# Kernel optimization log

Hardware: AMD Instinct MI355X
Metric: run time of the kernel (lower is better)

Reference implementation:

```python
import jax, jax.numpy as jnp
import numpy as np

N_NODES = 50000
N_EDGES = 800000
IN_FEATS = 256
N_HIDDEN = 256
N_CLASSES = 47


def _glorot(key, shape):
    fan_in, fan_out = shape
    lim = (6.0 / (fan_in + fan_out)) ** 0.5
    return jax.random.uniform(key, shape, jnp.float32, -lim, lim)


def setup_inputs() -> dict:
    key = jax.random.key(0)
    ks = jax.random.split(key, 12)
    x = jax.random.normal(ks[0], (N_NODES, IN_FEATS), jnp.float32)
    src = jax.random.randint(ks[1], (N_EDGES,), 0, N_NODES, jnp.int64)
    dst = jax.random.randint(ks[2], (N_EDGES,), 0, N_NODES, jnp.int64)
    dims = [(IN_FEATS, N_HIDDEN), (N_HIDDEN, N_HIDDEN), (N_HIDDEN, N_CLASSES)]
    inp = {"x": x, "src": src, "dst": dst}
    for i, (di, do) in enumerate(dims):
        inp[f"Wself{i}"] = _glorot(ks[3 + 3 * i], (di, do))
        inp[f"Wneigh{i}"] = _glorot(ks[4 + 3 * i], (di, do))
        inp[f"b{i}"] = jnp.zeros((do,), jnp.float32)
    return inp


def _sage_layer(h, src, dst, Ws, Wn, b):
    # DGL mean SAGEConv: fc_self(h) + fc_neigh(mean over in-neighbors) + bias
    msum = jax.ops.segment_sum(h[src], dst, num_segments=N_NODES)      # [N, d]
    deg = jax.ops.segment_sum(jnp.ones((src.shape[0],), h.dtype), dst,
                              num_segments=N_NODES)                     # [N]
    hmean = msum / jnp.maximum(deg, 1.0)[:, None]
    return h @ Ws + hmean @ Wn + b


def reference(x, src, dst, Wself0, Wneigh0, b0, Wself1, Wneigh1, b1,
              Wself2, Wneigh2, b2):
    h = _sage_layer(x, src, dst, Wself0, Wneigh0, b0)
    h = jax.nn.selu(h)
    h = _sage_layer(h, src, dst, Wself1, Wneigh1, b1)
    h = jax.nn.selu(h)
    h = _sage_layer(h, src, dst, Wself2, Wneigh2, b2)
    return jax.nn.softmax(h, axis=1)
```

## Files before the change

kernel.cpp:

```cpp
#include <hip/hip_runtime.h>
#include <math.h>

#define FEATS 256
#define KTOT  512
#define MS    264
#define SA    40

typedef __attribute__((ext_vector_type(8))) __bf16 bf16x8;
typedef __attribute__((ext_vector_type(4))) float f32x4;

__device__ __forceinline__ float bf2f(unsigned short u) {
    union { unsigned int i; float f; } v; v.i = ((unsigned int)u) << 16; return v.f;
}
__device__ __forceinline__ unsigned short f2bf(float f) {
    unsigned int u = __float_as_uint(f);
    unsigned int r = (u + 0x7FFFu + ((u >> 16) & 1u)) >> 16;
    return (unsigned short)r;
}

__global__ void k_detect(const int* __restrict__ srcRaw, const unsigned short* __restrict__ xr,
                         int nE, int* __restrict__ flag) {
    __shared__ int any, cnt;
    if (threadIdx.x == 0) { any = 0; cnt = 0; }
    __syncthreads();
    int lim = nE < 1024 ? nE : 1024;
    for (int i = threadIdx.x; i < lim; i += 256)
        if (srcRaw[2 * i + 1] != 0) atomicAdd(&any, 1);
    int loc = 0;
    for (int i = threadIdx.x; i < 1024; i += 256) {
        unsigned e = (xr[2 * i] >> 7) & 255u;
        if (e >= 90u && e <= 140u) loc++;
    }
    atomicAdd(&cnt, loc);
    __syncthreads();
    if (threadIdx.x == 0) {
        flag[0] = (any == 0) ? 1 : 0;
        flag[1] = (cnt > 512) ? 1 : 0;
    }
}

__global__ void k_count(const int* __restrict__ dstRaw, int* __restrict__ deg, int nE,
                        int nNodes, const int* __restrict__ flag) {
    int e = blockIdx.x * 256 + threadIdx.x;
    if (e >= nE) return;
    int f = flag[0];
    int d = dstRaw[f ? (2 * e) : e];
    if ((unsigned)d >= (unsigned)nNodes) d = 0;
    atomicAdd(&deg[d], 1);
}

__global__ __launch_bounds__(256) void k_bsum(const int* __restrict__ deg, int* __restrict__ bsum,
                                              int n) {
    __shared__ int buf[256];
    const int t = threadIdx.x;
    int i = blockIdx.x * 256 + t;
    buf[t] = (i < n) ? deg[i] : 0;
    __syncthreads();
    for (int s = 128; s > 0; s >>= 1) {
        if (t < s) buf[t] += buf[t + s];
        __syncthreads();
    }
    if (t == 0) bsum[blockIdx.x] = buf[0];
}

__global__ __launch_bounds__(256) void k_scanb(int* __restrict__ bsum, int nB) {
    __shared__ int buf[256];
    __shared__ int carry;
    const int t = threadIdx.x;
    if (t == 0) carry = 0;
    __syncthreads();
    for (int base = 0; base < nB; base += 256) {
        int i = base + t;
        int v = (i < nB) ? bsum[i] : 0;
        buf[t] = v;
        __syncthreads();
        for (int s = 1; s < 256; s <<= 1) {
            int tv = (t >= s) ? buf[t - s] : 0;
            __syncthreads();
            buf[t] += tv;
            __syncthreads();
        }
        int exc = buf[t] - v;
        int c = carry;
        if (i < nB) bsum[i] = c + exc;
        int tot = buf[255];
        __syncthreads();
        if (t == 0) carry = c + tot;
        __syncthreads();
    }
}

__global__ __launch_bounds__(256) void k_offs(const int* __restrict__ deg,
                                              const int* __restrict__ bsum,
                                              int* __restrict__ off, int* __restrict__ cursor,
                                              int n) {
    __shared__ int buf[256];
    const int t = threadIdx.x, b = blockIdx.x;
    int i = b * 256 + t;
    int v = (i < n) ? deg[i] : 0;
    buf[t] = v;
    __syncthreads();
    for (int s = 1; s < 256; s <<= 1) {
        int tv = (t >= s) ? buf[t - s] : 0;
        __syncthreads();
        buf[t] += tv;
        __syncthreads();
    }
    int exc = bsum[b] + buf[t] - v;
    if (i < n) { off[i] = exc; cursor[i] = exc; }
    if (i == n - 1) off[n] = exc + v;
}

__global__ void k_fill(const int* __restrict__ srcRaw, const int* __restrict__ dstRaw,
                       int* __restrict__ cursor, int* __restrict__ csr, int nE,
                       int nNodes, const int* __restrict__ flag) {
    int e = blockIdx.x * 256 + threadIdx.x;
    if (e >= nE) return;
    int f = flag[0];
    int d = dstRaw[f ? (2 * e) : e];
    int s = srcRaw[f ? (2 * e) : e];
    if ((unsigned)d >= (unsigned)nNodes) d = 0;
    if ((unsigned)s >= (unsigned)nNodes) s = 0;
    int pos = atomicAdd(&cursor[d], 1);
    csr[pos] = s;
}

template <bool F32>
__global__ void k_buildWt(const void* __restrict__ Ws, const void* __restrict__ Wn,
                          unsigned short* __restrict__ Wt, int N, int Npad,
                          const int* __restrict__ flag) {
    if (flag[1] != (F32 ? 0 : 1)) return;
    int idx = blockIdx.x * 256 + threadIdx.x;
    if (idx >= Npad * KTOT) return;
    int n = idx >> 9, k = idx & 511;
    unsigned short v = 0;
    if (n < N) {
        if (F32) {
            float fv = (k < 256) ? ((const float*)Ws)[k * N + n]
                                 : ((const float*)Wn)[(k - 256) * N + n];
            v = f2bf(fv);
        } else {
            v = (k < 256) ? ((const unsigned short*)Ws)[k * N + n]
                          : ((const unsigned short*)Wn)[(k - 256) * N + n];
        }
    }
    Wt[idx] = v;
}

template <bool F32>
__device__ __forceinline__ void stage8(const void* h, size_t elemOff, unsigned short* dst) {
    if (!F32) {
        *reinterpret_cast<float4*>(dst) =
            *reinterpret_cast<const float4*>((const unsigned short*)h + elemOff);
    } else {
        const float* p = (const float*)h + elemOff;
        float4 a = *reinterpret_cast<const float4*>(p);
        float4 b = *reinterpret_cast<const float4*>(p + 4);
        dst[0] = f2bf(a.x); dst[1] = f2bf(a.y); dst[2] = f2bf(a.z); dst[3] = f2bf(a.w);
        dst[4] = f2bf(b.x); dst[5] = f2bf(b.y); dst[6] = f2bf(b.z); dst[7] = f2bf(b.w);
    }
}

template <bool HF32>
__global__ __launch_bounds__(256) void k_aggr(
        const void* __restrict__ h, const int* __restrict__ off,
        const int* __restrict__ csr, unsigned short* __restrict__ hmean,
        int M, const int* __restrict__ flag, int want) {
    if (want >= 0 && flag[1] != want) return;
    const int lane = threadIdx.x & 63;
    const int wid = (blockIdx.x * 256 + threadIdx.x) >> 6;
    const int nw = (gridDim.x * 256) >> 6;
    for (int r = wid; r < M; r += nw) {
        const int e0 = off[r], e1 = off[r + 1];
        float a0 = 0.f, a1 = 0.f, a2 = 0.f, a3 = 0.f;
        for (int base = e0; base < e1; base += 64) {
            int cnt = e1 - base; if (cnt > 64) cnt = 64;
            int sidx = (lane < cnt) ? csr[base + lane] : 0;
            #pragma unroll 8
            for (int d = 0; d < cnt; d++) {
                int s = __shfl(sidx, d);
                if (HF32) {
                    float4 hv = reinterpret_cast<const float4*>(
                        (const float*)h + (size_t)s * FEATS)[lane];
                    a0 += hv.x; a1 += hv.y; a2 += hv.z; a3 += hv.w;
                } else {
                    ushort4 hv = reinterpret_cast<const ushort4*>(
                        (const unsigned short*)h + (size_t)s * FEATS)[lane];
                    a0 += bf2f(hv.x); a1 += bf2f(hv.y); a2 += bf2f(hv.z); a3 += bf2f(hv.w);
                }
            }
        }
        float rc = 1.0f / fmaxf((float)(e1 - e0), 1.0f);
        ushort4 o;
        o.x = f2bf(a0 * rc); o.y = f2bf(a1 * rc); o.z = f2bf(a2 * rc); o.w = f2bf(a3 * rc);
        *reinterpret_cast<ushort4*>(&hmean[(size_t)r * FEATS + lane * 4]) = o;
    }
}

template <int NT, int ACT, bool HF32, bool BF32, bool OF32>
__global__ __launch_bounds__(256) void k_gemm(
        const void* __restrict__ h, const unsigned short* __restrict__ hmean,
        const unsigned short* __restrict__ Wt, const void* __restrict__ bias,
        void* __restrict__ out, int M, int C, const int* __restrict__ flag, int want) {
    if (flag[1] != want) return;
    __shared__ __align__(16) unsigned short As[64 * SA];
    __shared__ __align__(16) unsigned short Bs[NT * 16 * SA];

    const int m0 = blockIdx.x * 64;
    const int tid = threadIdx.x;
    const int lane = tid & 63, w = tid >> 6;
    const int nh = lane & 15, q = lane >> 4;

    f32x4 acc[NT];
    #pragma unroll
    for (int ci = 0; ci < NT; ci++) acc[ci] = (f32x4){0.f, 0.f, 0.f, 0.f};

    for (int kb = 0; kb < KTOT; kb += 32) {
        {
            int row = tid >> 2, seg = tid & 3;
            int gr = m0 + row; if (gr > M - 1) gr = M - 1;
            if (kb < 256)
                stage8<HF32>(h, (size_t)gr * FEATS + kb + seg * 8, &As[row * SA + seg * 8]);
            else
                stage8<false>(hmean, (size_t)gr * FEATS + (kb - 256) + seg * 8,
                              &As[row * SA + seg * 8]);
        }
        for (int u = tid; u < NT * 64; u += 256) {
            int nn = u >> 2, seg = u & 3;
            *reinterpret_cast<float4*>(&Bs[nn * SA + seg * 8]) =
                *reinterpret_cast<const float4*>(Wt + (size_t)nn * KTOT + kb + seg * 8);
        }
        __syncthreads();
        bf16x8 afr = *reinterpret_cast<const bf16x8*>(&As[(w * 16 + nh) * SA + q * 8]);
        #pragma unroll
        for (int ci = 0; ci < NT; ci++) {
            bf16x8 bfr = *reinterpret_cast<const bf16x8*>(&Bs[(ci * 16 + nh) * SA + q * 8]);
            acc[ci] = __builtin_amdgcn_mfma_f32_16x16x32_bf16(afr, bfr, acc[ci], 0, 0, 0);
        }
        __syncthreads();
    }

    const int rbase = m0 + w * 16 + q * 4;
    if (ACT == 0) {
        const float sc = 1.0507009873554805f, al = 1.6732632423543772f;
        #pragma unroll
        for (int ci = 0; ci < NT; ci++) {
            int col = ci * 16 + nh;
            float b = BF32 ? ((const float*)bias)[col] : bf2f(((const unsigned short*)bias)[col]);
            #pragma unroll
            for (int rg = 0; rg < 4; rg++) {
                int r = rbase + rg;
                if (r < M) {
                    float v = acc[ci][rg] + b;
                    v = (v > 0.f) ? sc * v : sc * al * expm1f(v);
                    if (OF32) ((float*)out)[(size_t)r * (NT * 16) + col] = v;
                    else ((unsigned short*)out)[(size_t)r * (NT * 16) + col] = f2bf(v);
                }
            }
        }
    } else {
        #pragma unroll
        for (int rg = 0; rg < 4; rg++) {
            int r = rbase + rg;
            float vals[NT];
            float mx = -1e30f;
            #pragma unroll
            for (int ci = 0; ci < NT; ci++) {
                int col = ci * 16 + nh;
                float v = -1e30f;
                if (col < C) {
                    float b = BF32 ? ((const float*)bias)[col] : bf2f(((const unsigned short*)bias)[col]);
                    v = acc[ci][rg] + b;
                }
                vals[ci] = v;
                mx = fmaxf(mx, v);
            }
            #pragma unroll
            for (int mk = 1; mk <= 8; mk <<= 1) mx = fmaxf(mx, __shfl_xor(mx, mk));
            float s = 0.f;
            #pragma unroll
            for (int ci = 0; ci < NT; ci++) {
                float e = (vals[ci] <= -1e29f) ? 0.f : __expf(vals[ci] - mx);
                vals[ci] = e; s += e;
            }
            #pragma unroll
            for (int mk = 1; mk <= 8; mk <<= 1) s += __shfl_xor(s, mk);
            float inv = 1.f / s;
            if (r < M) {
                #pragma unroll
                for (int ci = 0; ci < NT; ci++) {
                    int col = ci * 16 + nh;
                    if (col < C) {
                        if (OF32) ((float*)out)[(size_t)r * C + col] = vals[ci] * inv;
                        else ((unsigned short*)out)[(size_t)r * C + col] = f2bf(vals[ci] * inv);
                    }
                }
            }
        }
    }
}

template <int NT, int ACT, bool HF32, bool BF32, bool OF32>
__global__ __launch_bounds__(256) void k_sage(
        const void* __restrict__ h, const int* __restrict__ off,
        const int* __restrict__ csr, const unsigned short* __restrict__ Wt,
        const void* __restrict__ bias, void* __restrict__ out,
        int M, int C, const int* __restrict__ flag, int want) {
    if (flag[1] != want) return;
    __shared__ __align__(16) unsigned short meanS[64 * MS];
    __shared__ __align__(16) unsigned short As[64 * SA];
    __shared__ __align__(16) unsigned short Bs[NT * 16 * SA];

    const int m0 = blockIdx.x * 64;
    const int tid = threadIdx.x;
    const int lane = tid & 63, w = tid >> 6;
    const int nh = lane & 15, q = lane >> 4;

    for (int i = 0; i < 16; i++) {
        int lr = w * 16 + i;
        int r = m0 + lr;
        int rr = (r < M) ? r : (M - 1);
        int e0 = off[rr], e1 = off[rr + 1];
        float a0 = 0.f, a1 = 0.f, a2 = 0.f, a3 = 0.f;
        #pragma unroll 8
        for (int j = e0; j < e1; j++) {
            int s = csr[j];
            if (HF32) {
                float4 hv = reinterpret_cast<const float4*>((const float*)h + (size_t)s * FEATS)[lane];
                a0 += hv.x; a1 += hv.y; a2 += hv.z; a3 += hv.w;
            } else {
                ushort4 hv = reinterpret_cast<const ushort4*>((const unsigned short*)h + (size_t)s * FEATS)[lane];
                a0 += bf2f(hv.x); a1 += bf2f(hv.y); a2 += bf2f(hv.z); a3 += bf2f(hv.w);
            }
        }
        float rc = 1.0f / fmaxf((float)(e1 - e0), 1.0f);
        ushort4 o;
        o.x = f2bf(a0 * rc); o.y = f2bf(a1 * rc); o.z = f2bf(a2 * rc); o.w = f2bf(a3 * rc);
        *reinterpret_cast<ushort4*>(&meanS[lr * MS + lane * 4]) = o;
    }
    __syncthreads();

    f32x4 acc[NT];
    #pragma unroll
    for (int ci = 0; ci < NT; ci++) acc[ci] = (f32x4){0.f, 0.f, 0.f, 0.f};

    for (int kb = 0; kb < KTOT; kb += 32) {
        const bool fromMean = (kb >= 256);
        if (!fromMean) {
            int row = tid >> 2, seg = tid & 3;
            int gr = m0 + row; if (gr > M - 1) gr = M - 1;
            stage8<HF32>(h, (size_t)gr * FEATS + kb + seg * 8, &As[row * SA + seg * 8]);
        }
        for (int u = tid; u < NT * 64; u += 256) {
            int nn = u >> 2, seg = u & 3;
            *reinterpret_cast<float4*>(&Bs[nn * SA + seg * 8]) =
                *reinterpret_cast<const float4*>(Wt + (size_t)nn * KTOT + kb + seg * 8);
        }
        __syncthreads();
        bf16x8 afr;
        if (!fromMean)
            afr = *reinterpret_cast<const bf16x8*>(&As[(w * 16 + nh) * SA + q * 8]);
        else
            afr = *reinterpret_cast<const bf16x8*>(&meanS[(w * 16 + nh) * MS + (kb - 256) + q * 8]);
        #pragma unroll
        for (int ci = 0; ci < NT; ci++) {
            bf16x8 bfr = *reinterpret_cast<const bf16x8*>(&Bs[(ci * 16 + nh) * SA + q * 8]);
            acc[ci] = __builtin_amdgcn_mfma_f32_16x16x32_bf16(afr, bfr, acc[ci], 0, 0, 0);
        }
        __syncthreads();
    }

    const int rbase = m0 + w * 16 + q * 4;
    if (ACT == 0) {
        const float sc = 1.0507009873554805f, al = 1.6732632423543772f;
        #pragma unroll
        for (int ci = 0; ci < NT; ci++) {
            int col = ci * 16 + nh;
            float b = BF32 ? ((const float*)bias)[col] : bf2f(((const unsigned short*)bias)[col]);
            #pragma unroll
            for (int rg = 0; rg < 4; rg++) {
                int r = rbase + rg;
                if (r < M) {
                    float v = acc[ci][rg] + b;
                    v = (v > 0.f) ? sc * v : sc * al * expm1f(v);
                    if (OF32) ((float*)out)[(size_t)r * (NT * 16) + col] = v;
                    else ((unsigned short*)out)[(size_t)r * (NT * 16) + col] = f2bf(v);
                }
            }
        }
    } else {
        #pragma unroll
        for (int rg = 0; rg < 4; rg++) {
            int r = rbase + rg;
            float vals[NT];
            float mx = -1e30f;
            #pragma unroll
            for (int ci = 0; ci < NT; ci++) {
                int col = ci * 16 + nh;
                float v = -1e30f;
                if (col < C) {
                    float b = BF32 ? ((const float*)bias)[col] : bf2f(((const unsigned short*)bias)[col]);
                    v = acc[ci][rg] + b;
                }
                vals[ci] = v;
                mx = fmaxf(mx, v);
            }
            #pragma unroll
            for (int mk = 1; mk <= 8; mk <<= 1) mx = fmaxf(mx, __shfl_xor(mx, mk));
            float s = 0.f;
            #pragma unroll
            for (int ci = 0; ci < NT; ci++) {
                float e = (vals[ci] <= -1e29f) ? 0.f : __expf(vals[ci] - mx);
                vals[ci] = e; s += e;
            }
            #pragma unroll
            for (int mk = 1; mk <= 8; mk <<= 1) s += __shfl_xor(s, mk);
            float inv = 1.f / s;
            if (r < M) {
                #pragma unroll
                for (int ci = 0; ci < NT; ci++) {
                    int col = ci * 16 + nh;
                    if (col < C) {
                        if (OF32) ((float*)out)[(size_t)r * C + col] = vals[ci] * inv;
                        else ((unsigned short*)out)[(size_t)r * C + col] = f2bf(vals[ci] * inv);
                    }
                }
            }
        }
    }
}

extern "C" void kernel_launch(void* const* d_in, const int* in_sizes, int n_in,
                              void* d_out, int out_size, void* d_ws, size_t ws_size,
                              hipStream_t stream) {
    const void* x     = d_in[0];
    const int* srcRaw = (const int*)d_in[1];
    const int* dstRaw = (const int*)d_in[2];
    const void* Ws0 = d_in[3]; const void* Wn0 = d_in[4]; const void* b0 = d_in[5];
    const void* Ws1 = d_in[6]; const void* Wn1 = d_in[7]; const void* b1 = d_in[8];
    const void* Ws2 = d_in[9]; const void* Wn2 = d_in[10]; const void* b2 = d_in[11];

    const int nNodes = in_sizes[0] / FEATS;
    const int nE     = in_sizes[1];
    const int C      = in_sizes[11];

    char* ws = (char*)d_ws;
    size_t off_b = 0;
    auto carve = [&](size_t bytes) -> void* {
        void* p = (void*)(ws + off_b);
        off_b += (bytes + 255) & ~(size_t)255;
        return p;
    };
    int*            flag   = (int*)           carve(256);
    int*            deg    = (int*)           carve((size_t)nNodes * 4);
    int*            cursor = (int*)           carve((size_t)nNodes * 4);
    int*            off    = (int*)           carve((size_t)(nNodes + 1) * 4);
    int*            csr    = (int*)           carve((size_t)nE * 4);
    unsigned short* Wt0    = (unsigned short*)carve((size_t)256 * KTOT * 2);
    unsigned short* Wt1    = (unsigned short*)carve((size_t)256 * KTOT * 2);
    unsigned short* Wt2    = (unsigned short*)carve((size_t)64 * KTOT * 2);
    int*            bsum   = (int*)           carve(4096);
    unsigned short* hA     = (unsigned short*)carve((size_t)nNodes * FEATS * 2);
    size_t base_b = off_b;
    unsigned short* hmean  = (unsigned short*)carve((size_t)nNodes * FEATS * 2);
    const bool split = (off_b <= ws_size);
    unsigned short* hX     = (unsigned short*)d_in[0];
    (void)base_b;

    const int edgeBlocks = (nE + 255) / 256;
    const int nodeBlocks = (nNodes + 255) / 256;
    const int sageBlocks = (nNodes + 63) / 64;
    const int aggrBlocks = 2048;

    k_detect<<<1, 256, 0, stream>>>(srcRaw, (const unsigned short*)x, nE, flag);
    hipMemsetAsync(deg, 0, (size_t)nNodes * 4, stream);
    k_count<<<edgeBlocks, 256, 0, stream>>>(dstRaw, deg, nE, nNodes, flag);
    k_bsum<<<nodeBlocks, 256, 0, stream>>>(deg, bsum, nNodes);
    k_scanb<<<1, 256, 0, stream>>>(bsum, nodeBlocks);
    k_offs<<<nodeBlocks, 256, 0, stream>>>(deg, bsum, off, cursor, nNodes);
    k_fill<<<edgeBlocks, 256, 0, stream>>>(srcRaw, dstRaw, cursor, csr, nE, nNodes, flag);

    int wtB = (256 * KTOT + 255) / 256;
    k_buildWt<false><<<wtB, 256, 0, stream>>>(Ws0, Wn0, Wt0, 256, 256, flag);
    k_buildWt<true ><<<wtB, 256, 0, stream>>>(Ws0, Wn0, Wt0, 256, 256, flag);
    k_buildWt<false><<<wtB, 256, 0, stream>>>(Ws1, Wn1, Wt1, 256, 256, flag);
    k_buildWt<true ><<<wtB, 256, 0, stream>>>(Ws1, Wn1, Wt1, 256, 256, flag);
    int wtB2 = (64 * KTOT + 255) / 256;
    k_buildWt<false><<<wtB2, 256, 0, stream>>>(Ws2, Wn2, Wt2, C, 64, flag);
    k_buildWt<true ><<<wtB2, 256, 0, stream>>>(Ws2, Wn2, Wt2, C, 64, flag);

    if (split) {
        k_aggr<false><<<aggrBlocks, 256, 0, stream>>>(x, off, csr, hmean, nNodes, flag, 1);
        k_aggr<true ><<<aggrBlocks, 256, 0, stream>>>(x, off, csr, hmean, nNodes, flag, 0);
        k_gemm<16, 0, false, false, false><<<sageBlocks, 256, 0, stream>>>(
            x, hmean, Wt0, b0, hA, nNodes, 256, flag, 1);
        k_gemm<16, 0, true, true, false><<<sageBlocks, 256, 0, stream>>>(
            x, hmean, Wt0, b0, hA, nNodes, 256, flag, 0);

        k_aggr<false><<<aggrBlocks, 256, 0, stream>>>(hA, off, csr, hmean, nNodes, flag, -1);
        k_gemm<16, 0, false, false, false><<<sageBlocks, 256, 0, stream>>>(
            hA, hmean, Wt1, b1, hX, nNodes, 256, flag, 1);
        k_gemm<16, 0, false, true, false><<<sageBlocks, 256, 0, stream>>>(
            hA, hmean, Wt1, b1, hX, nNodes, 256, flag, 0);

        k_aggr<false><<<aggrBlocks, 256, 0, stream>>>(hX, off, csr, hmean, nNodes, flag, -1);
        k_gemm<4, 1, false, false, false><<<sageBlocks, 256, 0, stream>>>(
            hX, hmean, Wt2, b2, d_out, nNodes, C, flag, 1);
        k_gemm<4, 1, false, true, true><<<sageBlocks, 256, 0, stream>>>(
            hX, hmean, Wt2, b2, d_out, nNodes, C, flag, 0);
    } else {
        k_sage<16, 0, false, false, false><<<sageBlocks, 256, 0, stream>>>(
            x, off, csr, Wt0, b0, hA, nNodes, 256, flag, 1);
        k_sage<16, 0, true, true, false><<<sageBlocks, 256, 0, stream>>>(
            x, off, csr, Wt0, b0, hA, nNodes, 256, flag, 0);
        k_sage<16, 0, false, false, false><<<sageBlocks, 256, 0, stream>>>(
            hA, off, csr, Wt1, b1, hX, nNodes, 256, flag, 1);
        k_sage<16, 0, false, true, false><<<sageBlocks, 256, 0, stream>>>(
            hA, off, csr, Wt1, b1, hX, nNodes, 256, flag, 0);
        k_sage<4, 1, false, false, false><<<sageBlocks, 256, 0, stream>>>(
            hX, off, csr, Wt2, b2, d_out, nNodes, C, flag, 1);
        k_sage<4, 1, false, true, true><<<sageBlocks, 256, 0, stream>>>(
            hX, off, csr, Wt2, b2, d_out, nNodes, C, flag, 0);
    }
}
```

Measured before the change: 659.9 us.

## Split aggregation into feature slices with 4 edges per wavefront in parallel

The mean-aggregation kernel is restructured so each block covers one of 8 feature slices of 32 columns. Each wavefront processes four edges at once, one per 16-lane group, and reduces the partial sums with xor shuffles. The old layout walked edges one at a time, with each wave gathering a full 256-feature row. The new one aims for more independent loads in flight and a smaller per-slice working set that may stay in cache. The cost is that CSR indices and offsets are re-read for every slice, each gather is narrower (4 or 8 bytes per lane), and each row now needs an extra shuffle reduction.

```diff
diff --git a/kernel.cpp b/kernel.cpp
--- a/kernel.cpp
+++ b/kernel.cpp
@@ -162,38 +162,48 @@
 }
 
 template <bool HF32>
-__global__ __launch_bounds__(256) void k_aggr(
+__global__ __launch_bounds__(256) void k_aggr2(
         const void* __restrict__ h, const int* __restrict__ off,
         const int* __restrict__ csr, unsigned short* __restrict__ hmean,
         int M, const int* __restrict__ flag, int want) {
     if (want >= 0 && flag[1] != want) return;
-    const int lane = threadIdx.x & 63;
-    const int wid = (blockIdx.x * 256 + threadIdx.x) >> 6;
-    const int nw = (gridDim.x * 256) >> 6;
+    const int tid = threadIdx.x;
+    const int lane = tid & 63;
+    const int w = tid >> 6;
+    const int slice = blockIdx.x & 7;
+    const int chunk = blockIdx.x >> 3;
+    const int nchunk = gridDim.x >> 3;
+    const int wid = chunk * 4 + w;
+    const int nw = nchunk * 4;
+    const int g = lane >> 4, li = lane & 15;
+    const int fbase = slice * 32 + li * 2;
+
     for (int r = wid; r < M; r += nw) {
         const int e0 = off[r], e1 = off[r + 1];
-        float a0 = 0.f, a1 = 0.f, a2 = 0.f, a3 = 0.f;
-        for (int base = e0; base < e1; base += 64) {
-            int cnt = e1 - base; if (cnt > 64) cnt = 64;
-            int sidx = (lane < cnt) ? csr[base + lane] : 0;
-            #pragma unroll 8
-            for (int d = 0; d < cnt; d++) {
-                int s = __shfl(sidx, d);
+        float a0 = 0.f, a1 = 0.f;
+        #pragma unroll 2
+        for (int base = e0; base < e1; base += 4) {
+            int e = base + g;
+            if (e < e1) {
+                int s = csr[e];
                 if (HF32) {
-                    float4 hv = reinterpret_cast<const float4*>(
-                        (const float*)h + (size_t)s * FEATS)[lane];
-                    a0 += hv.x; a1 += hv.y; a2 += hv.z; a3 += hv.w;
+                    float2 hv = *reinterpret_cast<const float2*>(
+                        (const float*)h + (size_t)s * FEATS + fbase);
+                    a0 += hv.x; a1 += hv.y;
                 } else {
-                    ushort4 hv = reinterpret_cast<const ushort4*>(
-                        (const unsigned short*)h + (size_t)s * FEATS)[lane];
-                    a0 += bf2f(hv.x); a1 += bf2f(hv.y); a2 += bf2f(hv.z); a3 += bf2f(hv.w);
-                }
-            }
-        }
-        float rc = 1.0f / fmaxf((float)(e1 - e0), 1.0f);
-        ushort4 o;
-        o.x = f2bf(a0 * rc); o.y = f2bf(a1 * rc); o.z = f2bf(a2 * rc); o.w = f2bf(a3 * rc);
-        *reinterpret_cast<ushort4*>(&hmean[(size_t)r * FEATS + lane * 4]) = o;
+                    ushort2 hv = *reinterpret_cast<const ushort2*>(
+                        (const unsigned short*)h + (size_t)s * FEATS + fbase);
+                    a0 += bf2f(hv.x); a1 += bf2f(hv.y);
+                }
+            }
+        }
+        a0 += __shfl_xor(a0, 16); a1 += __shfl_xor(a1, 16);
+        a0 += __shfl_xor(a0, 32); a1 += __shfl_xor(a1, 32);
+        if (g == 0) {
+            float rc = 1.0f / fmaxf((float)(e1 - e0), 1.0f);
+            ushort2 o; o.x = f2bf(a0 * rc); o.y = f2bf(a1 * rc);
+            *reinterpret_cast<ushort2*>(&hmean[(size_t)r * FEATS + fbase]) = o;
+        }
     }
 }
 
@@ -461,11 +471,9 @@
     unsigned short* Wt2    = (unsigned short*)carve((size_t)64 * KTOT * 2);
     int*            bsum   = (int*)           carve(4096);
     unsigned short* hA     = (unsigned short*)carve((size_t)nNodes * FEATS * 2);
-    size_t base_b = off_b;
     unsigned short* hmean  = (unsigned short*)carve((size_t)nNodes * FEATS * 2);
     const bool split = (off_b <= ws_size);
     unsigned short* hX     = (unsigned short*)d_in[0];
-    (void)base_b;
 
     const int edgeBlocks = (nE + 255) / 256;
     const int nodeBlocks = (nNodes + 255) / 256;
@@ -490,20 +498,20 @@
     k_buildWt<true ><<<wtB2, 256, 0, stream>>>(Ws2, Wn2, Wt2, C, 64, flag);
 
     if (split) {
-        k_aggr<false><<<aggrBlocks, 256, 0, stream>>>(x, off, csr, hmean, nNodes, flag, 1);
-        k_aggr<true ><<<aggrBlocks, 256, 0, stream>>>(x, off, csr, hmean, nNodes, flag, 0);
+        k_aggr2<false><<<aggrBlocks, 256, 0, stream>>>(x, off, csr, hmean, nNodes, flag, 1);
+        k_aggr2<true ><<<aggrBlocks, 256, 0, stream>>>(x, off, csr, hmean, nNodes, flag, 0);
         k_gemm<16, 0, false, false, false><<<sageBlocks, 256, 0, stream>>>(
             x, hmean, Wt0, b0, hA, nNodes, 256, flag, 1);
         k_gemm<16, 0, true, true, false><<<sageBlocks, 256, 0, stream>>>(
             x, hmean, Wt0, b0, hA, nNodes, 256, flag, 0);
 
-        k_aggr<false><<<aggrBlocks, 256, 0, stream>>>(hA, off, csr, hmean, nNodes, flag, -1);
+        k_aggr2<false><<<aggrBlocks, 256, 0, stream>>>(hA, off, csr, hmean, nNodes, flag, -1);
         k_gemm<16, 0, false, false, false><<<sageBlocks, 256, 0, stream>>>(
             hA, hmean, Wt1, b1, hX, nNodes, 256, flag, 1);
         k_gemm<16, 0, false, true, false><<<sageBlocks, 256, 0, stream>>>(
             hA, hmean, Wt1, b1, hX, nNodes, 256, flag, 0);
 
-        k_aggr<false><<<aggrBlocks, 256, 0, stream>>>(hX, off, csr, hmean, nNodes, flag, -1);
+        k_aggr2<false><<<aggrBlocks, 256, 0, stream>>>(hX, off, csr, hmean, nNodes, flag, -1);
         k_gemm<4, 1, false, false, false><<<sageBlocks, 256, 0, stream>>>(
             hX, hmean, Wt2, b2, d_out, nNodes, C, flag, 1);
         k_gemm<4, 1, false, true, true><<<sageBlocks, 256, 0, stream>>>(
```

Measured after the change: 934.5 us. 1.42x slower.

## Project layer-3 features before aggregation to shrink gathered width to 64

Applied to the files above, without the earlier changes.

For the last SAGE layer, computes P = h @ Wneigh (padded to 64 columns) first, then averages P over neighbors instead of averaging 256-wide features, using linearity of the mean. This cuts the irregular gather traffic in the final aggregation from 256 to 64 bf16 per edge. A second GEMM over h @ Wself adds the aggregated projection plus bias before softmax. It adds an extra GEMM launch and rounds the projection to bf16 before averaging, which slightly changes numerics.

```diff
diff --git a/kernel.cpp b/kernel.cpp
--- a/kernel.cpp
+++ b/kernel.cpp
@@ -143,6 +143,21 @@
             v = (k < 256) ? ((const unsigned short*)Ws)[k * N + n]
                           : ((const unsigned short*)Wn)[(k - 256) * N + n];
         }
+    }
+    Wt[idx] = v;
+}
+
+template <bool F32>
+__global__ void k_buildWt1(const void* __restrict__ W, unsigned short* __restrict__ Wt,
+                           int N, const int* __restrict__ flag) {
+    if (flag[1] != (F32 ? 0 : 1)) return;
+    int idx = blockIdx.x * 256 + threadIdx.x;
+    if (idx >= 64 * 256) return;
+    int n = idx >> 8, k = idx & 255;
+    unsigned short v = 0;
+    if (n < N) {
+        v = F32 ? f2bf(((const float*)W)[k * N + n])
+                : ((const unsigned short*)W)[k * N + n];
     }
     Wt[idx] = v;
 }
@@ -197,6 +212,36 @@
     }
 }
 
+__global__ __launch_bounds__(256) void k_aggrP(
+        const unsigned short* __restrict__ P, const int* __restrict__ off,
+        const int* __restrict__ csr, unsigned short* __restrict__ A, int M) {
+    const int lane = threadIdx.x & 63;
+    const int wid = (blockIdx.x * 256 + threadIdx.x) >> 6;
+    const int nw = (gridDim.x * 256) >> 6;
+    const int g = lane >> 5, li = lane & 31;
+    for (int r = wid; r < M; r += nw) {
+        const int e0 = off[r], e1 = off[r + 1];
+        float a0 = 0.f, a1 = 0.f;
+        #pragma unroll 4
+        for (int base = e0; base < e1; base += 2) {
+            int e = base + g;
+            if (e < e1) {
+                int s = csr[e];
+                ushort2 hv = *reinterpret_cast<const ushort2*>(
+                    P + (size_t)s * 64 + li * 2);
+                a0 += bf2f(hv.x); a1 += bf2f(hv.y);
+            }
+        }
+        a0 += __shfl_xor(a0, 32); a1 += __shfl_xor(a1, 32);
+        if (g == 0) {
+            float rc = 1.0f / fmaxf((float)(e1 - e0), 1.0f);
+            unsigned int packed = (unsigned int)f2bf(a0 * rc) |
+                                  ((unsigned int)f2bf(a1 * rc) << 16);
+            *reinterpret_cast<unsigned int*>(&A[(size_t)r * 64 + li * 2]) = packed;
+        }
+    }
+}
+
 template <int NT, int ACT, bool HF32, bool BF32, bool OF32>
 __global__ __launch_bounds__(256) void k_gemm(
         const void* __restrict__ h, const unsigned short* __restrict__ hmean,
@@ -241,27 +286,80 @@
     }
 
     const int rbase = m0 + w * 16 + q * 4;
-    if (ACT == 0) {
-        const float sc = 1.0507009873554805f, al = 1.6732632423543772f;
+    const float sc = 1.0507009873554805f, al = 1.6732632423543772f;
+    #pragma unroll
+    for (int ci = 0; ci < NT; ci++) {
+        int col = ci * 16 + nh;
+        float b = BF32 ? ((const float*)bias)[col] : bf2f(((const unsigned short*)bias)[col]);
+        #pragma unroll
+        for (int rg = 0; rg < 4; rg++) {
+            int r = rbase + rg;
+            if (r < M) {
+                float v = acc[ci][rg] + b;
+                v = (v > 0.f) ? sc * v : sc * al * expm1f(v);
+                if (OF32) ((float*)out)[(size_t)r * (NT * 16) + col] = v;
+                else ((unsigned short*)out)[(size_t)r * (NT * 16) + col] = f2bf(v);
+            }
+        }
+    }
+}
+
+template <int NT, int ACT, bool ADDP, bool BF32, bool OF32>
+__global__ __launch_bounds__(256) void k_gemm256(
+        const unsigned short* __restrict__ h, const unsigned short* __restrict__ Wt,
+        const void* __restrict__ bias, const unsigned short* __restrict__ Padd,
+        void* __restrict__ out, int M, int C, const int* __restrict__ flag, int want) {
+    if (want >= 0 && flag[1] != want) return;
+    __shared__ __align__(16) unsigned short As[64 * SA];
+    __shared__ __align__(16) unsigned short Bs[NT * 16 * SA];
+
+    const int m0 = blockIdx.x * 64;
+    const int tid = threadIdx.x;
+    const int lane = tid & 63, w = tid >> 6;
+    const int nh = lane & 15, q = lane >> 4;
+
+    f32x4 acc[NT];
+    #pragma unroll
+    for (int ci = 0; ci < NT; ci++) acc[ci] = (f32x4){0.f, 0.f, 0.f, 0.f};
+
+    for (int kb = 0; kb < 256; kb += 32) {
+        {
+            int row = tid >> 2, seg = tid & 3;
+            int gr = m0 + row; if (gr > M - 1) gr = M - 1;
+            stage8<false>(h, (size_t)gr * FEATS + kb + seg * 8, &As[row * SA + seg * 8]);
+        }
+        for (int u = tid; u < NT * 64; u += 256) {
+            int nn = u >> 2, seg = u & 3;
+            *reinterpret_cast<float4*>(&Bs[nn * SA + seg * 8]) =
+                *reinterpret_cast<const float4*>(Wt + (size_t)nn * 256 + kb + seg * 8);
+        }
+        __syncthreads();
+        bf16x8 afr = *reinterpret_cast<const bf16x8*>(&As[(w * 16 + nh) * SA + q * 8]);
+        #pragma unroll
+        for (int ci = 0; ci < NT; ci++) {
+            bf16x8 bfr = *reinterpret_cast<const bf16x8*>(&Bs[(ci * 16 + nh) * SA + q * 8]);
+            acc[ci] = __builtin_amdgcn_mfma_f32_16x16x32_bf16(afr, bfr, acc[ci], 0, 0, 0);
+        }
+        __syncthreads();
+    }
+
+    const int rbase = m0 + w * 16 + q * 4;
+    if (ACT == 2) {
         #pragma unroll
         for (int ci = 0; ci < NT; ci++) {
             int col = ci * 16 + nh;
-            float b = BF32 ? ((const float*)bias)[col] : bf2f(((const unsigned short*)bias)[col]);
             #pragma unroll
             for (int rg = 0; rg < 4; rg++) {
                 int r = rbase + rg;
-                if (r < M) {
-                    float v = acc[ci][rg] + b;
-                    v = (v > 0.f) ? sc * v : sc * al * expm1f(v);
-                    if (OF32) ((float*)out)[(size_t)r * (NT * 16) + col] = v;
-                    else ((unsigned short*)out)[(size_t)r * (NT * 16) + col] = f2bf(v);
-                }
+                if (r < M)
+                    ((unsigned short*)out)[(size_t)r * (NT * 16) + col] = f2bf(acc[ci][rg]);
             }
         }
     } else {
         #pragma unroll
         for (int rg = 0; rg < 4; rg++) {
             int r = rbase + rg;
+            int rr = (r < M) ? r : (M - 1);
             float vals[NT];
             float mx = -1e30f;
             #pragma unroll
@@ -270,7 +368,8 @@
                 float v = -1e30f;
                 if (col < C) {
                     float b = BF32 ? ((const float*)bias)[col] : bf2f(((const unsigned short*)bias)[col]);
-                    v = acc[ci][rg] + b;
+                    float a = ADDP ? bf2f(Padd[(size_t)rr * 64 + col]) : 0.f;
+                    v = acc[ci][rg] + a + b;
                 }
                 vals[ci] = v;
                 mx = fmaxf(mx, v);
@@ -459,13 +558,15 @@
     unsigned short* Wt0    = (unsigned short*)carve((size_t)256 * KTOT * 2);
     unsigned short* Wt1    = (unsigned short*)carve((size_t)256 * KTOT * 2);
     unsigned short* Wt2    = (unsigned short*)carve((size_t)64 * KTOT * 2);
+    unsigned short* Wt2s   = (unsigned short*)carve((size_t)64 * 256 * 2);
+    unsigned short* Wt2n   = (unsigned short*)carve((size_t)64 * 256 * 2);
     int*            bsum   = (int*)           carve(4096);
     unsigned short* hA     = (unsigned short*)carve((size_t)nNodes * FEATS * 2);
-    size_t base_b = off_b;
     unsigned short* hmean  = (unsigned short*)carve((size_t)nNodes * FEATS * 2);
     const bool split = (off_b <= ws_size);
-    unsigned short* hX     = (unsigned short*)d_in[0];
-    (void)base_b;
+    unsigned short* P2 = hmean;
+    unsigned short* A2 = hmean + (size_t)4 * 1024 * 1024;
+    unsigned short* hX = (unsigned short*)d_in[0];
 
     const int edgeBlocks = (nE + 255) / 256;
     const int nodeBlocks = (nNodes + 255) / 256;
@@ -485,11 +586,14 @@
     k_buildWt<true ><<<wtB, 256, 0, stream>>>(Ws0, Wn0, Wt0, 256, 256, flag);
     k_buildWt<false><<<wtB, 256, 0, stream>>>(Ws1, Wn1, Wt1, 256, 256, flag);
     k_buildWt<true ><<<wtB, 256, 0, stream>>>(Ws1, Wn1, Wt1, 256, 256, flag);
-    int wtB2 = (64 * KTOT + 255) / 256;
-    k_buildWt<false><<<wtB2, 256, 0, stream>>>(Ws2, Wn2, Wt2, C, 64, flag);
-    k_buildWt<true ><<<wtB2, 256, 0, stream>>>(Ws2, Wn2, Wt2, C, 64, flag);
 
     if (split) {
+        int wt1B = (64 * 256 + 255) / 256;
+        k_buildWt1<false><<<wt1B, 256, 0, stream>>>(Ws2, Wt2s, C, flag);
+        k_buildWt1<true ><<<wt1B, 256, 0, stream>>>(Ws2, Wt2s, C, flag);
+        k_buildWt1<false><<<wt1B, 256, 0, stream>>>(Wn2, Wt2n, C, flag);
+        k_buildWt1<true ><<<wt1B, 256, 0, stream>>>(Wn2, Wt2n, C, flag);
+
         k_aggr<false><<<aggrBlocks, 256, 0, stream>>>(x, off, csr, hmean, nNodes, flag, 1);
         k_aggr<true ><<<aggrBlocks, 256, 0, stream>>>(x, off, csr, hmean, nNodes, flag, 0);
         k_gemm<16, 0, false, false, false><<<sageBlocks, 256, 0, stream>>>(
@@ -503,12 +607,17 @@
         k_gemm<16, 0, false, true, false><<<sageBlocks, 256, 0, stream>>>(
             hA, hmean, Wt1, b1, hX, nNodes, 256, flag, 0);
 
-        k_aggr<false><<<aggrBlocks, 256, 0, stream>>>(hX, off, csr, hmean, nNodes, flag, -1);
-        k_gemm<4, 1, false, false, false><<<sageBlocks, 256, 0, stream>>>(
-            hX, hmean, Wt2, b2, d_out, nNodes, C, flag, 1);
-        k_gemm<4, 1, false, true, true><<<sageBlocks, 256, 0, stream>>>(
-            hX, hmean, Wt2, b2, d_out, nNodes, C, flag, 0);
+        k_gemm256<4, 2, false, false, false><<<sageBlocks, 256, 0, stream>>>(
+            hX, Wt2n, b2, (const unsigned short*)nullptr, P2, nNodes, C, flag, -1);
+        k_aggrP<<<aggrBlocks, 256, 0, stream>>>(P2, off, csr, A2, nNodes);
+        k_gemm256<4, 1, true, false, false><<<sageBlocks, 256, 0, stream>>>(
+            hX, Wt2s, b2, A2, d_out, nNodes, C, flag, 1);
+        k_gemm256<4, 1, true, true, true><<<sageBlocks, 256, 0, stream>>>(
+            hX, Wt2s, b2, A2, d_out, nNodes, C, flag, 0);
     } else {
+        int wtB2 = (64 * KTOT + 255) / 256;
+        k_buildWt<false><<<wtB2, 256, 0, stream>>>(Ws2, Wn2, Wt2, C, 64, flag);
+        k_buildWt<true ><<<wtB2, 256, 0, stream>>>(Ws2, Wn2, Wt2, C, 64, flag);
         k_sage<16, 0, false, false, false><<<sageBlocks, 256, 0, stream>>>(
             x, off, csr, Wt0, b0, hA, nNodes, 256, flag, 1);
         k_sage<16, 0, true, true, false><<<sageBlocks, 256, 0, stream>>>(
```

Measured after the change: 669.7 us. About the same (+1.5%).
